# Optimization experiments

Measured on AMD Instinct MI355X. Metric: run time of the kernel, lower is better.

## Reference

```python
import jax, jax.numpy as jnp
import numpy as np

B, T_ENC, T_DEC = 64, 512, 400
IN_DIM, R = 80, 2
D_ENC, D_ATT, D_PRE = 256, 256, 128
NEG_INF = -1e9


def _gru(x, h, Wi, Wh, bi, bh):
    # PyTorch GRUCell math
    gi = x @ Wi + bi
    gh = h @ Wh + bh
    ir, iz, inn = jnp.split(gi, 3, axis=-1)
    hr, hz, hn = jnp.split(gh, 3, axis=-1)
    r = jax.nn.sigmoid(ir + hr)
    z = jax.nn.sigmoid(iz + hz)
    n = jnp.tanh(inn + r * hn)
    return (1.0 - z) * n + z * h


def setup_inputs() -> dict:
    key = jax.random.key(0)
    ks = jax.random.split(key, 32)
    s = 0.05
    d_in = IN_DIM * R
    inp = {
        "encoder_outputs": jax.random.normal(ks[0], (B, T_ENC, D_ENC), jnp.float32),
        "inputs": jax.random.normal(ks[1], (B, T_DEC, d_in), jnp.float32),
        "memory_lengths": jax.random.randint(ks[2], (B,), T_ENC // 2, T_ENC + 1).astype(jnp.int32),
        # prenet
        "pre_W1": s * jax.random.normal(ks[3], (d_in, 256), jnp.float32),
        "pre_b1": jnp.zeros((256,), jnp.float32),
        "pre_W2": s * jax.random.normal(ks[4], (256, 128), jnp.float32),
        "pre_b2": jnp.zeros((128,), jnp.float32),
        # Bahdanau attention
        "mem_W": s * jax.random.normal(ks[5], (D_ENC, D_ATT), jnp.float32),
        "q_W": s * jax.random.normal(ks[6], (256, D_ATT), jnp.float32),
        "v_W": s * jax.random.normal(ks[7], (D_ATT, 1), jnp.float32),
        # attention GRUCell: input = cat(prenet 128, attention 256) = 384
        "att_Wi": s * jax.random.normal(ks[8], (384, 768), jnp.float32),
        "att_Wh": s * jax.random.normal(ks[9], (256, 768), jnp.float32),
        "att_bi": jnp.zeros((768,), jnp.float32),
        "att_bh": jnp.zeros((768,), jnp.float32),
        # project_to_decoder_in
        "proj_in_W": s * jax.random.normal(ks[10], (512, 256), jnp.float32),
        "proj_in_b": jnp.zeros((256,), jnp.float32),
        # decoder GRUCells
        "dec1_Wi": s * jax.random.normal(ks[11], (256, 768), jnp.float32),
        "dec1_Wh": s * jax.random.normal(ks[12], (256, 768), jnp.float32),
        "dec1_bi": jnp.zeros((768,), jnp.float32),
        "dec1_bh": jnp.zeros((768,), jnp.float32),
        "dec2_Wi": s * jax.random.normal(ks[13], (256, 768), jnp.float32),
        "dec2_Wh": s * jax.random.normal(ks[14], (256, 768), jnp.float32),
        "dec2_bi": jnp.zeros((768,), jnp.float32),
        "dec2_bh": jnp.zeros((768,), jnp.float32),
        # output projections
        "mel_W": s * jax.random.normal(ks[15], (256, d_in), jnp.float32),
        "mel_b": jnp.zeros((d_in,), jnp.float32),
        "gate_W": s * jax.random.normal(ks[16], (256, R), jnp.float32),
        "gate_b": jnp.zeros((R,), jnp.float32),
    }
    return inp


def _decoder_forward(encoder_outputs, inputs, memory_lengths,
                     pre_W1, pre_b1, pre_W2, pre_b2,
                     mem_W, q_W, v_W,
                     att_Wi, att_Wh, att_bi, att_bh,
                     proj_in_W, proj_in_b,
                     dec1_Wi, dec1_Wh, dec1_bi, dec1_bh,
                     dec2_Wi, dec2_Wh, dec2_bi, dec2_bh,
                     mel_W, mel_b, gate_W, gate_b):
    Bq, Tq, _ = encoder_outputs.shape
    processed_memory = encoder_outputs @ mem_W  # (B, T_enc, D_att)
    valid = jnp.arange(Tq)[None, :] < memory_lengths[:, None]  # (B, T_enc)

    # teacher forcing: input at step t is inputs[t-1], zeros at t=0
    prev = jnp.concatenate([jnp.zeros_like(inputs[:, :1]), inputs[:, :-1]], axis=1)
    prev = jnp.swapaxes(prev, 0, 1)  # (T_dec, B, in_dim*r)

    def prenet(x):
        # dropout is identity in eval mode
        h = jax.nn.relu(x @ pre_W1 + pre_b1)
        return jax.nn.relu(h @ pre_W2 + pre_b2)

    def step(carry, x_prev):
        att_h, h1, h2, cur_att = carry
        pre = prenet(x_prev)  # (B, 128)
        cell_in = jnp.concatenate([pre, cur_att], axis=-1)  # (B, 384)
        att_h = _gru(cell_in, att_h, att_Wi, att_Wh, att_bi, att_bh)  # (B, 256)
        # Bahdanau alignment over encoder memory
        score = jnp.squeeze(
            jnp.tanh(processed_memory + (att_h @ q_W)[:, None, :]) @ v_W, -1)  # (B, T_enc)
        score = jnp.where(valid, score, NEG_INF)
        align = jax.nn.softmax(score, axis=-1)
        cur_att = jnp.einsum('bt,btd->bd', align, encoder_outputs)  # (B, 256)
        dec_in = jnp.concatenate([att_h, cur_att], axis=-1) @ proj_in_W + proj_in_b
        h1 = _gru(dec_in, h1, dec1_Wi, dec1_Wh, dec1_bi, dec1_bh)
        d = h1 + dec_in
        h2 = _gru(d, h2, dec2_Wi, dec2_Wh, dec2_bi, dec2_bh)
        d = h2 + d
        gate = jax.nn.sigmoid(d @ gate_W + gate_b)  # (B, r)
        out = d @ mel_W + mel_b  # (B, in_dim*r)
        return (att_h, h1, h2, cur_att), (out, align, gate)

    z = jnp.zeros((Bq, 256), encoder_outputs.dtype)
    init = (z, z, z, z)
    _, (outs, aligns, gates) = jax.lax.scan(step, init, prev)
    outputs = jnp.swapaxes(outs, 0, 1)      # (B, T_dec, in_dim*r)
    alignments = jnp.swapaxes(aligns, 0, 1)  # (B, T_dec, T_enc)
    gates = jnp.swapaxes(gates, 0, 1)        # (B, T_dec, r)
    return outputs, alignments, gates


def reference(encoder_outputs, inputs, memory_lengths,
              pre_W1, pre_b1, pre_W2, pre_b2,
              mem_W, q_W, v_W,
              att_Wi, att_Wh, att_bi, att_bh,
              proj_in_W, proj_in_b,
              dec1_Wi, dec1_Wh, dec1_bi, dec1_bh,
              dec2_Wi, dec2_Wh, dec2_bi, dec2_bh,
              mel_W, mel_b, gate_W, gate_b):
    return _decoder_forward(encoder_outputs, inputs, memory_lengths,
                            pre_W1, pre_b1, pre_W2, pre_b2,
                            mem_W, q_W, v_W,
                            att_Wi, att_Wh, att_bi, att_bh,
                            proj_in_W, proj_in_b,
                            dec1_Wi, dec1_Wh, dec1_bi, dec1_bh,
                            dec2_Wi, dec2_Wh, dec2_bi, dec2_bh,
                            mel_W, mel_b, gate_W, gate_b)
```

## Files before the change

kernel.cpp:

```cpp
#include <hip/hip_runtime.h>

#define TDEC 400
#define NTH 512
#define NWG 256

typedef float f32x4 __attribute__((ext_vector_type(4)));
typedef unsigned u32x4 __attribute__((ext_vector_type(4)));
typedef unsigned u32x2 __attribute__((ext_vector_type(2)));

#define OFF_BAR   0
#define OFF_ATTH  11264
#define OFF_H1    44032
#define OFF_H2    76800
#define OFF_CURP  109568
#define OFF_ATTS  125952
#define OFF_Q     126208
#define ZERO_FLOATS 142592
#define OFF_D1    142592
#define OFF_SUMS  158976
#define OFF_C1    184576
#define OFF_PRE   185600
#define OFF_PMB   1824000
#define OFF_ENCB  6018304
#define OFF_D2A   10212608
#define T_WIT_A   10212608
#define T_WHT_A   10507520
#define T_M1T     10704128
#define T_WHT1    11097344
#define T_PJT     11293952
#define T_WIT2    11425024
#define T_WHT2    11621632
#define T_QWT     11818240
#define T_M1      11883776
#define OFF_BLOB  16766208

#define BLOB_N   26112
#define BLOB_STR 26624
#define BO_AI  0
#define BO_AH  4608
#define BO_Q   7680
#define BO_M1  8704
#define BO_H1  14848
#define BO_PJ  17920
#define BO_I2  19968
#define BO_H2  23040

#define AOFF 4096000
#define GOFF 17203200

#define MSTI  (8*1024)
#define GENI  (9*1024)
#define FAILI (10*1024)

__device__ __forceinline__ float fsig(float x){ return 1.0f/(1.0f+__expf(-x)); }
__device__ __forceinline__ float ftanh(float x){ float e = __expf(2.0f*x); return 1.0f - 2.0f/(e+1.0f); }
__device__ __forceinline__ float blo(unsigned u){ return __uint_as_float(u<<16); }
__device__ __forceinline__ float bhi(unsigned u){ return __uint_as_float(u & 0xffff0000u); }

__device__ __forceinline__ f32x4 cload16(const float* p){
  f32x4 r;
  asm volatile("global_load_dwordx4 %0, %1, off sc0 sc1" : "=v"(r) : "v"(p));
  return r;
}
__device__ __forceinline__ u32x4 cload16u(const unsigned short* p){
  u32x4 r;
  asm volatile("global_load_dwordx4 %0, %1, off sc0 sc1" : "=v"(r) : "v"(p));
  return r;
}
__device__ __forceinline__ float aload4(const float* p){
  unsigned u = __hip_atomic_load((const unsigned*)p, __ATOMIC_RELAXED, __HIP_MEMORY_SCOPE_AGENT);
  return __uint_as_float(u);
}
__device__ __forceinline__ void astore4(float* p, float v){
  __hip_atomic_store((unsigned*)p, __float_as_uint(v), __ATOMIC_RELAXED, __HIP_MEMORY_SCOPE_AGENT);
}
__device__ __forceinline__ void aadd(float* p, float v){
  __hip_atomic_fetch_add(p, v, __ATOMIC_RELAXED, __HIP_MEMORY_SCOPE_AGENT);
}
__device__ __forceinline__ int aloadi(const int* p){
  return __hip_atomic_load(p, __ATOMIC_RELAXED, __HIP_MEMORY_SCOPE_AGENT);
}

__device__ __forceinline__ void ldsbar(){
  __builtin_amdgcn_sched_barrier(0);
  asm volatile("s_waitcnt lgkmcnt(0)" ::: "memory");
  __builtin_amdgcn_s_barrier();
  __builtin_amdgcn_sched_barrier(0);
}

__device__ __forceinline__ void gbar(int* bar, int g, int l, int n){
  asm volatile("s_waitcnt vmcnt(0)" ::: "memory");
  __syncthreads();
  if (threadIdx.x == 0){
    if (aloadi(&bar[FAILI]) == 0){
      int a = __hip_atomic_fetch_add(&bar[(l&7)*1024 + g*64], 1, __ATOMIC_RELAXED, __HIP_MEMORY_SCOPE_AGENT);
      if (a == 8*n - 1){
        int m = __hip_atomic_fetch_add(&bar[MSTI + g*64], 1, __ATOMIC_RELAXED, __HIP_MEMORY_SCOPE_AGENT);
        if (m == 8*n - 1)
          __hip_atomic_store(&bar[GENI + g*64], n, __ATOMIC_RELAXED, __HIP_MEMORY_SCOPE_AGENT);
      }
      int sp = 0;
      while (aloadi(&bar[GENI + g*64]) < n){
        __builtin_amdgcn_s_sleep(1);
        if (++sp > (1<<20)){
          __hip_atomic_store(&bar[FAILI], 1, __ATOMIC_RELAXED, __HIP_MEMORY_SCOPE_AGENT);
          break;
        }
      }
    }
  }
  __syncthreads();
}

__device__ __forceinline__ unsigned short f2bf(float f){
  unsigned u = __float_as_uint(f);
  return (unsigned short)((u + 0x7fffu + ((u>>16)&1u)) >> 16);
}

template<int N8>
__device__ __forceinline__ float bdot(const unsigned short* wr, const float* xr){
  f32x4 accA = 0.f, accB = 0.f;
  #pragma unroll 4
  for (int k = 0; k < N8; ++k){
    u32x4 u = *(const u32x4*)(wr + k*8);
    f32x4 a = *(const f32x4*)(xr + k*8);
    f32x4 b = *(const f32x4*)(xr + k*8 + 4);
    f32x4 w0, w1;
    w0[0]=blo(u[0]); w0[1]=bhi(u[0]); w0[2]=blo(u[1]); w0[3]=bhi(u[1]);
    w1[0]=blo(u[2]); w1[1]=bhi(u[2]); w1[2]=blo(u[3]); w1[3]=bhi(u[3]);
    accA += w0*a; accB += w1*b;
  }
  f32x4 s = accA + accB;
  return s[0]+s[1]+s[2]+s[3];
}

__global__ __launch_bounds__(256, 1) void transpose_k(const float* __restrict__ in,
                                                      float* __restrict__ outp, int K, int C){
  __shared__ float tl[32][33];
  int c0 = blockIdx.x * 32, k0 = blockIdx.y * 32;
  int tx = threadIdx.x & 31, ty = threadIdx.x >> 5;
  for (int i = ty; i < 32; i += 8){
    int k = k0 + i, c = c0 + tx;
    if (k < K && c < C) tl[i][tx] = in[k * C + c];
  }
  __syncthreads();
  for (int i = ty; i < 32; i += 8){
    int c = c0 + i, k = k0 + tx;
    if (c < C && k < K) outp[c * K + k] = tl[tx][i];
  }
}

__global__ __launch_bounds__(128, 1) void fuse_k(const float* __restrict__ projW,
    const float* __restrict__ d1Wi, float* __restrict__ M1){
  int jt = blockIdx.x % 6, i = blockIdx.x / 6;
  int j = jt * 128 + threadIdx.x;
  float acc = 0.f;
  for (int k = 0; k < 256; ++k) acc += projW[i*256+k] * d1Wi[k*768+j];
  M1[i*768+j] = acc;
}

__global__ __launch_bounds__(256, 1) void c1_k(const float* __restrict__ projB,
    const float* __restrict__ d1Wi, const float* __restrict__ d1Bi, float* __restrict__ C1){
  int j = blockIdx.x * 256 + threadIdx.x;
  float acc = d1Bi[j];
  for (int k = 0; k < 256; ++k) acc += projB[k] * d1Wi[k*768+j];
  C1[j] = acc;
}

__global__ __launch_bounds__(512, 1) void pack_k(float* __restrict__ ws){
  int sl = blockIdx.x;
  const float* TAI = ws + T_WIT_A;
  const float* TAH = ws + T_WHT_A;
  const float* TM1 = ws + T_M1T;
  const float* TH1 = ws + T_WHT1;
  const float* TPJ = ws + T_PJT;
  const float* TI2 = ws + T_WIT2;
  const float* TH2 = ws + T_WHT2;
  const float* TQ  = ws + T_QWT;
  unsigned short* blob = (unsigned short*)(ws + OFF_BLOB) + (size_t)sl * BLOB_STR;
  for (int idx = threadIdx.x; idx < BLOB_N; idx += 512){
    float v; int cs, k, o;
    if (idx < BO_AH){ cs = idx / 384; k = idx - cs*384;
      v = TAI[((cs%3)*256 + sl*4 + cs/3)*384 + k]; }
    else if (idx < BO_Q){ o = idx - BO_AH; cs = o >> 8; k = o & 255;
      v = TAH[((cs%3)*256 + sl*4 + cs/3)*256 + k]; }
    else if (idx < BO_M1){ o = idx - BO_Q; cs = o >> 8; k = o & 255;
      v = TQ[(sl*4 + cs)*256 + k]; }
    else if (idx < BO_H1){ o = idx - BO_M1; cs = o >> 9; k = o & 511;
      v = TM1[((cs%3)*256 + sl*4 + cs/3)*512 + k]; }
    else if (idx < BO_PJ){ o = idx - BO_H1; cs = o >> 8; k = o & 255;
      v = TH1[((cs%3)*256 + sl*4 + cs/3)*256 + k]; }
    else if (idx < BO_I2){ o = idx - BO_PJ; cs = o >> 9; k = o & 511;
      v = TPJ[(sl*4 + cs)*512 + k]; }
    else if (idx < BO_H2){ o = idx - BO_I2; cs = o >> 8; k = o & 255;
      v = TI2[((cs%3)*256 + sl*4 + cs/3)*256 + k]; }
    else { o = idx - BO_H2; cs = o >> 8; k = o & 255;
      v = TH2[((cs%3)*256 + sl*4 + cs/3)*256 + k]; }
    blob[idx] = f2bf(v);
  }
}

__global__ __launch_bounds__(256, 1) void qt_k(const float* __restrict__ ws,
                                               float* __restrict__ out){
  unsigned short* qtb = (unsigned short*)(out + GOFF);
  const float* TQ = ws + T_QWT;
  int idx = blockIdx.x * 256 + threadIdx.x;
  int it = idx >> 11, j = (idx >> 3) & 255, e = idx & 7;
  qtb[idx] = f2bf(TQ[j*256 + it*8 + e]);
}

__global__ __launch_bounds__(NTH, 1) void prenet_k(float* __restrict__ ws,
    const float* __restrict__ inp, const float* __restrict__ W1, const float* __restrict__ B1,
    const float* __restrict__ W2, const float* __restrict__ B2){
  __shared__ float xT[160 * 33];
  __shared__ float hT[256 * 33];
  int t = blockIdx.x, half = blockIdx.y, tid = threadIdx.x;
  int bbase = half * 32;
  for (int r = tid; r < 32 * 160; r += NTH){
    int b2 = r / 160; int k = r - b2 * 160;
    xT[k * 33 + b2] = (t == 0) ? 0.f : inp[((bbase + b2) * TDEC + (t - 1)) * 160 + k];
  }
  __syncthreads();
  int bl = tid & 31, slot = tid >> 5;
  float acc1[16];
  #pragma unroll
  for (int i = 0; i < 16; ++i) acc1[i] = 0.f;
  for (int k = 0; k < 160; ++k){
    float xv = xT[k * 33 + bl];
    const float* wr = W1 + k * 256 + slot * 16;
    #pragma unroll
    for (int i = 0; i < 16; ++i) acc1[i] += xv * wr[i];
  }
  #pragma unroll
  for (int i = 0; i < 16; ++i){
    int c = slot * 16 + i;
    hT[c * 33 + bl] = fmaxf(acc1[i] + B1[c], 0.f);
  }
  __syncthreads();
  float acc2[8];
  #pragma unroll
  for (int i = 0; i < 8; ++i) acc2[i] = 0.f;
  for (int k = 0; k < 256; ++k){
    float hv = hT[k * 33 + bl];
    const float* wr = W2 + k * 128 + slot * 8;
    #pragma unroll
    for (int i = 0; i < 8; ++i) acc2[i] += hv * wr[i];
  }
  unsigned short* dst = (unsigned short*)(ws + OFF_PRE) + (size_t)t*8192 + (bbase + bl)*128 + slot*8;
  u32x4 pk;
  #pragma unroll
  for (int i = 0; i < 4; ++i){
    float v0 = fmaxf(acc2[2*i] + B2[slot*8 + 2*i], 0.f);
    float v1 = fmaxf(acc2[2*i+1] + B2[slot*8 + 2*i+1], 0.f);
    pk[i] = (unsigned)f2bf(v0) | ((unsigned)f2bf(v1) << 16);
  }
  *(u32x4*)dst = pk;
}

__global__ __launch_bounds__(NTH, 1) void pm_k(float* __restrict__ ws,
    const float* __restrict__ enc, const float* __restrict__ memW){
  int wg = blockIdx.x, tid = threadIdx.x;
  int b = wg & 63, th = wg >> 6;
  int slot = tid & 7, tt = tid >> 3;
  int trow = th * 64 + tt;
  const float* er = enc + ((size_t)(b * 512 + trow)) * 256;
  f32x4 acc[8];
  #pragma unroll
  for (int i = 0; i < 8; ++i) acc[i] = 0.f;
  for (int k = 0; k < 256; ++k){
    float ev = er[k];
    const f32x4* wr = (const f32x4*)(memW + k * 256 + slot * 32);
    #pragma unroll
    for (int i = 0; i < 8; ++i) acc[i] += ev * wr[i];
  }
  unsigned short* pmB = (unsigned short*)(ws + OFF_PMB);
  unsigned short* dst = pmB + ((size_t)(b * 512 + trow)) * 256 + slot * 32;
  #pragma unroll
  for (int i = 0; i < 8; ++i){
    u32x2 pk;
    pk[0] = (unsigned)f2bf(acc[i][0]) | ((unsigned)f2bf(acc[i][1]) << 16);
    pk[1] = (unsigned)f2bf(acc[i][2]) | ((unsigned)f2bf(acc[i][3]) << 16);
    *(u32x2*)(dst + i * 4) = pk;
  }
  const float* e2 = enc + ((size_t)(b * 512 + th * 64)) * 256;
  unsigned* eb = (unsigned*)((unsigned short*)(ws + OFF_ENCB) + ((size_t)(b * 512 + th * 64)) * 256);
  for (int i = tid; i < 64 * 128; i += NTH){
    float v0 = e2[i * 2], v1 = e2[i * 2 + 1];
    eb[i] = (unsigned)f2bf(v0) | ((unsigned)f2bf(v1) << 16);
  }
}

__global__ __launch_bounds__(NTH, 2) void decoder_k(
    float* __restrict__ ws, float* __restrict__ out,
    const int* __restrict__ memlen,
    const float* __restrict__ vW,
    const float* __restrict__ attBi, const float* __restrict__ attBh,
    const float* __restrict__ projB,
    const float* __restrict__ d1Bh,
    const float* __restrict__ d2Bi, const float* __restrict__ d2Bh)
{
  const int wg = blockIdx.x, tid = threadIdx.x;
  int* bar = (int*)ws;
  float* attH = ws + OFF_ATTH;
  float* h1a  = ws + OFF_H1;
  float* h2a  = ws + OFF_H2;
  float* const curB[2]  = { ws + OFF_CURP, ws + OFF_Q };
  float* const attSB[2] = { ws + OFF_ATTS, ws + OFF_ATTS + 64 };
  float* d1v  = ws + OFF_D1;
  const float* C1v = ws + OFF_C1;
  const unsigned short* preB16 = (const unsigned short*)(ws + OFF_PRE);
  const unsigned short* pmB  = (const unsigned short*)(ws + OFF_PMB);
  const unsigned short* encB = (const unsigned short*)(ws + OFF_ENCB);
  const unsigned short* qtb = (const unsigned short*)(out + GOFF);
  float* d2a  = ws + OFF_D2A;

  __shared__ float POOL[16128];
  float* const ahL  = POOL;
  float* const cnL  = POOL + 4160;
  float* const h1L  = POOL + 8320;
  float* const xpre = POOL + 12480;
  float* const dL   = POOL;
  float* const h2L  = POOL + 4160;
  float* const ctxP = POOL + 8320;
  float* const qIn  = POOL + 12416;
  float* const ewGi  = POOL + 14592;
  float* const ewGh  = POOL + 14784;
  float* const ewGi2 = POOL + 14976;
  float* const ewGh2 = POOL + 15168;
  float* const pdec  = POOL + 15360;
  float* const qL    = POOL + 15488;
  float* const vL    = POOL + 15744;
  float* const eL    = POOL + 16000;

  if (tid < 256) vL[tid] = vW[tid];

  const int g = wg >> 6, l = wg & 63;
  const int sl = l;
  const int b0 = g << 4;
  const int b2 = b0 + (l >> 2), ch2 = l & 3;
  const int len2 = memlen[b2];
  const unsigned short* blob = (const unsigned short*)(ws + OFF_BLOB) + (size_t)sl * BLOB_STR;

  const int bq = tid & 15, x = tid >> 4;
  const int cs = (x >= 12 && x < 24) ? (x - 12) : x;
  const int gg = cs % 3, jh = cs / 3;
  const int col = gg * 256 + sl * 4 + jh;

  const int r0 = tid >> 6, c0 = (tid & 63) << 2;
  const int r1 = r0 + 8;
  const int prr = tid >> 4, pcc = (tid & 15) * 8;

  float rb0 = 0.f, rb1 = 0.f, rb2 = 0.f;
  if (x < 12){ rb0 = attBi[col]; rb1 = C1v[col];  rb2 = d2Bi[col]; }
  else if (x < 24){ rb0 = attBh[col]; rb1 = d1Bh[col]; rb2 = d2Bh[col]; }
  float pjB2 = 0.f;
  if (tid >= 64 && tid < 128) pjB2 = projB[sl*4 + ((tid - 64) >> 4)];

  u32x4 pmv[8], env[8];
  {
    int te = tid >> 2, part = tid & 3;
    const u32x4* pmp = (const u32x4*)(pmB + ((size_t)(b2*512 + ch2*128 + te))*256 + part*64);
    #pragma unroll
    for (int i = 0; i < 8; ++i) pmv[i] = pmp[i];
    int ich = tid >> 5, dblk = tid & 31;
    const unsigned short* ep = encB + ((size_t)(b2*512 + ch2*128 + ich*8))*256 + dblk*8;
    #pragma unroll
    for (int i = 0; i < 8; ++i) env[i] = *(const u32x4*)(ep + i*256);
  }

  f32x4 eA0, eA1, eH0, eH1;
  u32x4 ppre = 0u;
  eA0 = cload16(attH + 16384 + ((b0+r0)<<8) + c0);
  eA1 = cload16(attH + 16384 + ((b0+r1)<<8) + c0);
  eH0 = cload16(h1a + ((b0+r0)<<8) + c0);
  eH1 = cload16(h1a + ((b0+r1)<<8) + c0);
  if (tid < 256) ppre = cload16u(preB16 + (b0 + prr)*128 + pcc);

  int bn = 0;
  for (int t = -1; t <= 400; ++t){
    const int w = t & 1, wn = w ^ 1;

    if (t >= 0){
      const bool doP2 = (t < 400), doP5 = (t >= 1);
      f32x4 vD0 = cload16(d1v + ((b0+r0)<<8) + c0);
      f32x4 vD1 = cload16(d1v + ((b0+r1)<<8) + c0);
      f32x4 vH0 = cload16(h2a + w*16384 + ((b0+r0)<<8) + c0);
      f32x4 vH1 = cload16(h2a + w*16384 + ((b0+r1)<<8) + c0);
      f32x4 qv = 0.f;
      if (tid < 64) qv = cload16(attH + w*16384 + b2*256 + tid*4);
      eA0 = cload16(attH + w*16384 + ((b0+r0)<<8) + c0);
      eA1 = cload16(attH + w*16384 + ((b0+r1)<<8) + c0);
      eH0 = cload16(h1a + wn*16384 + ((b0+r0)<<8) + c0);
      eH1 = cload16(h1a + wn*16384 + ((b0+r1)<<8) + c0);
      {
        int tn = (t + 1 < TDEC) ? (t + 1) : (TDEC - 1);
        if (tid < 256) ppre = cload16u(preB16 + (size_t)tn*8192 + (b0 + prr)*128 + pcc);
      }
      asm volatile("s_waitcnt vmcnt(0)" : "+v"(vD0),"+v"(vD1),"+v"(vH0),"+v"(vH1),"+v"(qv));
      __builtin_amdgcn_sched_barrier(0);
      if (tid < 64) *(f32x4*)(qIn + tid*4) = qv;
      *(f32x4*)(dL + r0*260 + c0) = vD0;  *(f32x4*)(dL + r1*260 + c0) = vD1;
      *(f32x4*)(h2L + r0*260 + c0) = vH0; *(f32x4*)(h2L + r1*260 + c0) = vH1;
      ldsbar();
      if (doP2){
        int lane = tid & 63;
        int j = (tid >> 6)*32 + (lane & 31), hf = lane >> 5;
        const unsigned short* qw = qtb + j*8 + (size_t)hf*32768;
        const float* qx = qIn + hf*128;
        f32x4 aA = 0.f, aB = 0.f;
        #pragma unroll 4
        for (int it = 0; it < 16; ++it){
          u32x4 u = *(const u32x4*)(qw + (size_t)it*2048);
          f32x4 a = *(const f32x4*)(qx + it*8);
          f32x4 b = *(const f32x4*)(qx + it*8 + 4);
          f32x4 w0, w1;
          w0[0]=blo(u[0]); w0[1]=bhi(u[0]); w0[2]=blo(u[1]); w0[3]=bhi(u[1]);
          w1[0]=blo(u[2]); w1[1]=bhi(u[2]); w1[2]=blo(u[3]); w1[3]=bhi(u[3]);
          aA += w0*a; aB += w1*b;
        }
        f32x4 s4 = aA + aB;
        float s = s4[0]+s4[1]+s4[2]+s4[3];
        s += __shfl_xor(s, 32);
        if (hf == 0) qL[j] = s;
      }
      if (doP5){
        if (x < 12)
          ewGi[cs*16 + bq] = bdot<32>(blob + BO_I2 + cs*256, dL + bq*260) + rb2;
        else if (x < 24)
          ewGh[cs*16 + bq] = bdot<32>(blob + BO_H2 + cs*256, h2L + bq*260) + rb2;
      }
      ldsbar();
      if (doP2){
        int te = tid >> 2, part = tid & 3;
        int ge = ch2*128 + te;
        float a4 = 0.f;
        #pragma unroll
        for (int i = 0; i < 8; ++i){
          u32x4 u = pmv[i];
          int kb = part*64 + i*8;
          a4 += ftanh(blo(u[0]) + qL[kb+0]) * vL[kb+0];
          a4 += ftanh(bhi(u[0]) + qL[kb+1]) * vL[kb+1];
          a4 += ftanh(blo(u[1]) + qL[kb+2]) * vL[kb+2];
          a4 += ftanh(bhi(u[1]) + qL[kb+3]) * vL[kb+3];
          a4 += ftanh(blo(u[2]) + qL[kb+4]) * vL[kb+4];
          a4 += ftanh(bhi(u[2]) + qL[kb+5]) * vL[kb+5];
          a4 += ftanh(blo(u[3]) + qL[kb+6]) * vL[kb+6];
          a4 += ftanh(bhi(u[3]) + qL[kb+7]) * vL[kb+7];
        }
        a4 += __shfl_xor(a4, 1);
        a4 += __shfl_xor(a4, 2);
        float e = (ge < len2) ? __expf(a4) : 0.f;
        if (part == 0){
          eL[te] = e;
          out[AOFF + ((size_t)(b2*TDEC + t))*512 + ge] = e;
        }
      }
      if (doP5 && tid < 64){
        int bt = tid & 15, jj = tid >> 4;
        int j = sl*4 + jj;
        float ir = ewGi[(jj*3+0)*16+bt] + ewGh[(jj*3+0)*16+bt];
        float iz = ewGi[(jj*3+1)*16+bt] + ewGh[(jj*3+1)*16+bt];
        float inn = ewGi[(jj*3+2)*16+bt];
        float hn  = ewGh[(jj*3+2)*16+bt];
        float rg = fsig(ir), z = fsig(iz);
        float n = ftanh(inn + rg * hn);
        float hv = h2L[bt*260 + j];
        float hnew = (1.f - z)*n + z*hv;
        astore4(h2a + wn*16384 + (b0+bt)*256 + j, hnew);
        d2a[(size_t)(t-1)*16384 + j*64 + (b0+bt)] = hnew + dL[bt*260 + j];
      }
      ldsbar();
      if (doP2){
        if (tid < 64){
          float s = eL[tid] + eL[tid + 64];
          #pragma unroll
          for (int o = 32; o > 0; o >>= 1) s += __shfl_down(s, o);
          if (tid == 0) aadd(attSB[w] + b2, s);
        }
        {
          int ich = tid >> 5, dblk = tid & 31;
          f32x4 acA = 0.f, acB = 0.f;
          #pragma unroll
          for (int i = 0; i < 8; ++i){
            u32x4 u = env[i];
            float e = eL[ich*8 + i];
            acA[0] += e*blo(u[0]); acA[1] += e*bhi(u[0]);
            acA[2] += e*blo(u[1]); acA[3] += e*bhi(u[1]);
            acB[0] += e*blo(u[2]); acB[1] += e*bhi(u[2]);
            acB[2] += e*blo(u[3]); acB[3] += e*bhi(u[3]);
          }
          *(f32x4*)(ctxP + tid*8) = acA;
          *(f32x4*)(ctxP + tid*8 + 4) = acB;
        }
      }
      ldsbar();
      if (doP2 && tid < 256){
        int dblk = tid >> 3, d = tid & 7;
        float s = 0.f;
        #pragma unroll
        for (int i = 0; i < 16; ++i) s += ctxP[i*256 + dblk*8 + d];
        aadd(curB[w] + b2*256 + dblk*8 + d, s);
      }
    }

    gbar(bar, g, l, ++bn);
    if (t == 400) break;

    {
      const bool doP0 = (t <= 398), doP4 = (t >= 0);
      f32x4 vC0 = cload16(curB[w] + ((b0+r0)<<8) + c0);
      f32x4 vC1 = cload16(curB[w] + ((b0+r1)<<8) + c0);
      float s0 = aload4(attSB[w] + b0 + r0), s1 = aload4(attSB[w] + b0 + r1);
      asm volatile("s_waitcnt vmcnt(0)" : "+v"(vC0),"+v"(vC1));
      __builtin_amdgcn_sched_barrier(0);
      float iv0 = s0 > 0.f ? 1.f/s0 : 0.f, iv1 = s1 > 0.f ? 1.f/s1 : 0.f;
      *(f32x4*)(ahL + r0*260 + c0) = eA0; *(f32x4*)(ahL + r1*260 + c0) = eA1;
      *(f32x4*)(h1L + r0*260 + c0) = eH0; *(f32x4*)(h1L + r1*260 + c0) = eH1;
      *(f32x4*)(cnL + r0*260 + c0) = vC0*iv0; *(f32x4*)(cnL + r1*260 + c0) = vC1*iv1;
      if (tid < 256){
        float* xd = xpre + prr*132 + pcc;
        xd[0]=blo(ppre[0]); xd[1]=bhi(ppre[0]); xd[2]=blo(ppre[1]); xd[3]=bhi(ppre[1]);
        xd[4]=blo(ppre[2]); xd[5]=bhi(ppre[2]); xd[6]=blo(ppre[3]); xd[7]=bhi(ppre[3]);
      }
      if (tid < 64) astore4(curB[wn] + wg*64 + tid, 0.f);
      if (sl == 0 && tid < 16) astore4(attSB[wn] + b0 + tid, 0.f);
      if (t >= 0 && sl == 0 && tid < 16)
        ws[OFF_SUMS + t*64 + b0 + tid] = aload4(attSB[w] + b0 + tid);
      ldsbar();
      if (x < 12){
        if (doP0)
          ewGi[cs*16 + bq] = bdot<16>(blob + BO_AI + cs*384, xpre + bq*132)
                           + bdot<32>(blob + BO_AI + cs*384 + 128, cnL + bq*260) + rb0;
        if (doP4)
          ewGi2[cs*16 + bq] = bdot<32>(blob + BO_M1 + cs*512, ahL + bq*260)
                            + bdot<32>(blob + BO_M1 + cs*512 + 256, cnL + bq*260) + rb1;
      } else if (x < 24){
        if (doP0)
          ewGh[cs*16 + bq] = bdot<32>(blob + BO_AH + cs*256, ahL + bq*260) + rb0;
        if (doP4)
          ewGh2[cs*16 + bq] = bdot<32>(blob + BO_H1 + cs*256, h1L + bq*260) + rb1;
      } else if (doP4){
        int idx = tid - 384;
        int bq2 = idx & 15, cc = (idx >> 4) & 3, half = idx >> 6;
        pdec[idx] = bdot<32>(blob + BO_PJ + cc*512 + half*256, (half ? cnL : ahL) + bq2*260);
      }
      ldsbar();
      if (doP0 && tid < 64){
        int bt = tid & 15, jj = tid >> 4;
        int j = sl*4 + jj;
        float ir = ewGi[(jj*3+0)*16+bt] + ewGh[(jj*3+0)*16+bt];
        float iz = ewGi[(jj*3+1)*16+bt] + ewGh[(jj*3+1)*16+bt];
        float inn = ewGi[(jj*3+2)*16+bt];
        float hn  = ewGh[(jj*3+2)*16+bt];
        float rg = fsig(ir), z = fsig(iz);
        float n = ftanh(inn + rg * hn);
        float h = ahL[bt*260 + j];
        astore4(attH + wn*16384 + (b0+bt)*256 + j, (1.f - z)*n + z*h);
      }
      if (doP4 && tid >= 64 && tid < 128){
        int t2 = tid - 64;
        int bt = t2 & 15, jj = t2 >> 4;
        int j = sl*4 + jj;
        float ir = ewGi2[(jj*3+0)*16+bt] + ewGh2[(jj*3+0)*16+bt];
        float iz = ewGi2[(jj*3+1)*16+bt] + ewGh2[(jj*3+1)*16+bt];
        float inn = ewGi2[(jj*3+2)*16+bt];
        float hn  = ewGh2[(jj*3+2)*16+bt];
        float rg = fsig(ir), z = fsig(iz);
        float n = ftanh(inn + rg * hn);
        float hv = h1L[bt*260 + j];
        float hnew = (1.f - z)*n + z*hv;
        float dec = pdec[jj*16 + bt] + pdec[64 + jj*16 + bt] + pjB2;
        astore4(h1a + w*16384 + (b0+bt)*256 + j, hnew);
        astore4(d1v + (b0+bt)*256 + j, hnew + dec);
      }
    }
    gbar(bar, g, l, ++bn);
  }
}

__global__ __launch_bounds__(NTH, 1) void rescale_k(const float* __restrict__ ws,
                                                    float* __restrict__ out){
  int blk = blockIdx.x;
  int b = blk / TDEC, t = blk - b * TDEC;
  float s = ws[OFF_SUMS + t*64 + b];
  float inv = (s > 0.f) ? 1.f/s : 0.f;
  out[AOFF + (size_t)blk*512 + threadIdx.x] *= inv;
}

__global__ __launch_bounds__(NTH, 1) void outproj_k(const float* __restrict__ ws,
    float* __restrict__ out, const float* __restrict__ melW, const float* __restrict__ melB,
    const float* __restrict__ gateW, const float* __restrict__ gateB){
  int t = blockIdx.x, tid = threadIdx.x;
  int cx = tid & 255, bh = tid >> 8;
  const float* src = ws + OFF_D2A + t*16384 + bh*32;
  float acc[32];
  #pragma unroll
  for (int i = 0; i < 32; ++i) acc[i] = 0.f;
  bool ismel = (cx < 160);
  bool isgate = (cx >= 160 && cx < 162);
  for (int j = 0; j < 256; ++j){
    float wv = 0.f;
    if (ismel) wv = melW[j*160 + cx];
    else if (isgate) wv = gateW[j*2 + (cx - 160)];
    const f32x4* dp = (const f32x4*)(src + j*64);
    f32x4 vv[8];
    #pragma unroll
    for (int q = 0; q < 8; ++q) vv[q] = dp[q];
    #pragma unroll
    for (int q = 0; q < 8; ++q){
      acc[q*4+0] += vv[q][0]*wv; acc[q*4+1] += vv[q][1]*wv;
      acc[q*4+2] += vv[q][2]*wv; acc[q*4+3] += vv[q][3]*wv;
    }
  }
  if (ismel){
    float bb = melB[cx];
    #pragma unroll
    for (int i = 0; i < 32; ++i){
      int b = bh*32 + i;
      out[((size_t)(b*TDEC + t))*160 + cx] = acc[i] + bb;
    }
  } else if (isgate){
    int g = cx - 160;
    float bb = gateB[g];
    #pragma unroll
    for (int i = 0; i < 32; ++i){
      int b = bh*32 + i;
      out[GOFF + ((size_t)(b*TDEC + t))*2 + g] = fsig(acc[i] + bb);
    }
  }
}

extern "C" void kernel_launch(void* const* d_in, const int* in_sizes, int n_in,
                              void* d_out, int out_size, void* d_ws, size_t ws_size,
                              hipStream_t stream)
{
  (void)in_sizes; (void)n_in; (void)out_size; (void)ws_size;
  const float* enc   = (const float*)d_in[0];
  const float* inp   = (const float*)d_in[1];
  const int*   mlen  = (const int*)d_in[2];
  const float* preW1 = (const float*)d_in[3];
  const float* preB1 = (const float*)d_in[4];
  const float* preW2 = (const float*)d_in[5];
  const float* preB2 = (const float*)d_in[6];
  const float* memW  = (const float*)d_in[7];
  const float* qW    = (const float*)d_in[8];
  const float* vW    = (const float*)d_in[9];
  const float* attWi = (const float*)d_in[10];
  const float* attWh = (const float*)d_in[11];
  const float* attBi = (const float*)d_in[12];
  const float* attBh = (const float*)d_in[13];
  const float* projW = (const float*)d_in[14];
  const float* projB = (const float*)d_in[15];
  const float* d1Wi  = (const float*)d_in[16];
  const float* d1Wh  = (const float*)d_in[17];
  const float* d1Bi  = (const float*)d_in[18];
  const float* d1Bh  = (const float*)d_in[19];
  const float* d2Wi  = (const float*)d_in[20];
  const float* d2Wh  = (const float*)d_in[21];
  const float* d2Bi  = (const float*)d_in[22];
  const float* d2Bh  = (const float*)d_in[23];
  const float* melW  = (const float*)d_in[24];
  const float* melB  = (const float*)d_in[25];
  const float* gateW = (const float*)d_in[26];
  const float* gateB = (const float*)d_in[27];
  float* ws = (float*)d_ws;
  float* out = (float*)d_out;

  hipMemsetAsync(d_ws, 0, (size_t)ZERO_FLOATS * sizeof(float), stream);

  dim3 tt(256);
  transpose_k<<<dim3(24, 12), tt, 0, stream>>>(attWi, ws + T_WIT_A, 384, 768);
  transpose_k<<<dim3(24, 8),  tt, 0, stream>>>(attWh, ws + T_WHT_A, 256, 768);
  transpose_k<<<dim3(24, 8),  tt, 0, stream>>>(d1Wh,  ws + T_WHT1, 256, 768);
  transpose_k<<<dim3(24, 8),  tt, 0, stream>>>(d2Wi,  ws + T_WIT2, 256, 768);
  transpose_k<<<dim3(24, 8),  tt, 0, stream>>>(d2Wh,  ws + T_WHT2, 256, 768);
  transpose_k<<<dim3(8, 16),  tt, 0, stream>>>(projW, ws + T_PJT, 512, 256);
  transpose_k<<<dim3(8, 8),   tt, 0, stream>>>(qW,    ws + T_QWT, 256, 256);
  fuse_k<<<3072, 128, 0, stream>>>(projW, d1Wi, ws + T_M1);
  c1_k<<<3, 256, 0, stream>>>(projB, d1Wi, d1Bi, ws + OFF_C1);
  transpose_k<<<dim3(24, 16), tt, 0, stream>>>(ws + T_M1, ws + T_M1T, 512, 768);
  pack_k<<<64, NTH, 0, stream>>>(ws);
  qt_k<<<256, 256, 0, stream>>>(ws, out);

  prenet_k<<<dim3(TDEC, 2), NTH, 0, stream>>>(ws, inp, preW1, preB1, preW2, preB2);
  pm_k<<<512, NTH, 0, stream>>>(ws, enc, memW);
  decoder_k<<<NWG, NTH, 0, stream>>>(ws, out, mlen, vW, attBi, attBh, projB,
                                     d1Bh, d2Bi, d2Bh);
  rescale_k<<<64 * TDEC, NTH, 0, stream>>>(ws, out);
  outproj_k<<<TDEC, NTH, 0, stream>>>(ws, out, melW, melB, gateW, gateB);
}
```

Before: 12.02 ms.

## Restructure grid barrier into 16 counters with leader flag polling, cache query weights in registers

Replaces the two-level grid barrier (8 counters plus a master counter) with 16 per-slice counters. Each counter sets a flag, and a single leader workgroup polls all 16 flags before publishing the generation. This is meant to shorten the serial atomic chain on the critical path of the persistent kernel's per-step barrier. The query-projection weights are also preloaded once into registers instead of being reloaded every timestep, and the prenet loads drop the cache-bypass bits. The cost is 64 more VGPRs per thread, which risks spills or lower occupancy, and barrier latency now depends on one leader workgroup.

Result: slower. 23.68 ms (+97.0%).

```diff
diff --git a/kernel.cpp b/kernel.cpp
--- a/kernel.cpp
+++ b/kernel.cpp
@@ -48,8 +48,8 @@
 #define AOFF 4096000
 #define GOFF 17203200
 
-#define MSTI  (8*1024)
-#define GENI  (9*1024)
+#define FLAGB (8*1024)
+#define GENIB 9728
 #define FAILI (10*1024)
 
 __device__ __forceinline__ float fsig(float x){ return 1.0f/(1.0f+__expf(-x)); }
@@ -62,9 +62,9 @@
   asm volatile("global_load_dwordx4 %0, %1, off sc0 sc1" : "=v"(r) : "v"(p));
   return r;
 }
-__device__ __forceinline__ u32x4 cload16u(const unsigned short* p){
+__device__ __forceinline__ u32x4 ncload16u(const unsigned short* p){
   u32x4 r;
-  asm volatile("global_load_dwordx4 %0, %1, off sc0 sc1" : "=v"(r) : "v"(p));
+  asm volatile("global_load_dwordx4 %0, %1, off" : "=v"(r) : "v"(p));
   return r;
 }
 __device__ __forceinline__ float aload4(const float* p){
@@ -79,6 +79,9 @@
 }
 __device__ __forceinline__ int aloadi(const int* p){
   return __hip_atomic_load(p, __ATOMIC_RELAXED, __HIP_MEMORY_SCOPE_AGENT);
+}
+__device__ __forceinline__ void astorei(int* p, int v){
+  __hip_atomic_store(p, v, __ATOMIC_RELAXED, __HIP_MEMORY_SCOPE_AGENT);
 }
 
 __device__ __forceinline__ void ldsbar(){
@@ -93,18 +96,33 @@
   __syncthreads();
   if (threadIdx.x == 0){
     if (aloadi(&bar[FAILI]) == 0){
-      int a = __hip_atomic_fetch_add(&bar[(l&7)*1024 + g*64], 1, __ATOMIC_RELAXED, __HIP_MEMORY_SCOPE_AGENT);
-      if (a == 8*n - 1){
-        int m = __hip_atomic_fetch_add(&bar[MSTI + g*64], 1, __ATOMIC_RELAXED, __HIP_MEMORY_SCOPE_AGENT);
-        if (m == 8*n - 1)
-          __hip_atomic_store(&bar[GENI + g*64], n, __ATOMIC_RELAXED, __HIP_MEMORY_SCOPE_AGENT);
-      }
-      int sp = 0;
-      while (aloadi(&bar[GENI + g*64]) < n){
-        __builtin_amdgcn_s_sleep(1);
-        if (++sp > (1<<20)){
-          __hip_atomic_store(&bar[FAILI], 1, __ATOMIC_RELAXED, __HIP_MEMORY_SCOPE_AGENT);
-          break;
+      int c = l & 15;
+      int a = __hip_atomic_fetch_add(&bar[c*512 + g*64], 1, __ATOMIC_RELAXED, __HIP_MEMORY_SCOPE_AGENT);
+      if (a == 4*n - 1)
+        astorei(&bar[FLAGB + g*64 + c], n);
+      if (l == 0){
+        int sp = 0;
+        for (;;){
+          int ok = 1;
+          #pragma unroll
+          for (int c2 = 0; c2 < 16; ++c2)
+            ok &= (aloadi(&bar[FLAGB + g*64 + c2]) >= n) ? 1 : 0;
+          if (ok) break;
+          __builtin_amdgcn_s_sleep(1);
+          if (++sp > (1<<20)){
+            astorei(&bar[FAILI], 1);
+            break;
+          }
+        }
+        astorei(&bar[GENIB + g*64], n);
+      } else {
+        int sp = 0;
+        while (aloadi(&bar[GENIB + g*64]) < n){
+          __builtin_amdgcn_s_sleep(1);
+          if (++sp > (1<<20)){
+            astorei(&bar[FAILI], 1);
+            break;
+          }
         }
       }
     }
@@ -356,7 +374,7 @@
   float pjB2 = 0.f;
   if (tid >= 64 && tid < 128) pjB2 = projB[sl*4 + ((tid - 64) >> 4)];
 
-  u32x4 pmv[8], env[8];
+  u32x4 pmv[8], env[8], qwv[16];
   {
     int te = tid >> 2, part = tid & 3;
     const u32x4* pmp = (const u32x4*)(pmB + ((size_t)(b2*512 + ch2*128 + te))*256 + part*64);
@@ -366,7 +384,14 @@
     const unsigned short* ep = encB + ((size_t)(b2*512 + ch2*128 + ich*8))*256 + dblk*8;
     #pragma unroll
     for (int i = 0; i < 8; ++i) env[i] = *(const u32x4*)(ep + i*256);
-  }
+    int lane = tid & 63;
+    int jq = (tid >> 6)*32 + (lane & 31), hfq = lane >> 5;
+    const unsigned short* qw = qtb + jq*8 + (size_t)hfq*32768;
+    #pragma unroll
+    for (int it = 0; it < 16; ++it) qwv[it] = *(const u32x4*)(qw + (size_t)it*2048);
+  }
+  const int qhf = (tid & 63) >> 5;
+  const int qj  = (tid >> 6)*32 + (tid & 31);
 
   f32x4 eA0, eA1, eH0, eH1;
   u32x4 ppre = 0u;
@@ -374,7 +399,7 @@
   eA1 = cload16(attH + 16384 + ((b0+r1)<<8) + c0);
   eH0 = cload16(h1a + ((b0+r0)<<8) + c0);
   eH1 = cload16(h1a + ((b0+r1)<<8) + c0);
-  if (tid < 256) ppre = cload16u(preB16 + (b0 + prr)*128 + pcc);
+  if (tid < 256) ppre = ncload16u(preB16 + (b0 + prr)*128 + pcc);
 
   int bn = 0;
   for (int t = -1; t <= 400; ++t){
@@ -394,7 +419,7 @@
       eH1 = cload16(h1a + wn*16384 + ((b0+r1)<<8) + c0);
       {
         int tn = (t + 1 < TDEC) ? (t + 1) : (TDEC - 1);
-        if (tid < 256) ppre = cload16u(preB16 + (size_t)tn*8192 + (b0 + prr)*128 + pcc);
+        if (tid < 256) ppre = ncload16u(preB16 + (size_t)tn*8192 + (b0 + prr)*128 + pcc);
       }
       asm volatile("s_waitcnt vmcnt(0)" : "+v"(vD0),"+v"(vD1),"+v"(vH0),"+v"(vH1),"+v"(qv));
       __builtin_amdgcn_sched_barrier(0);
@@ -403,14 +428,11 @@
       *(f32x4*)(h2L + r0*260 + c0) = vH0; *(f32x4*)(h2L + r1*260 + c0) = vH1;
       ldsbar();
       if (doP2){
-        int lane = tid & 63;
-        int j = (tid >> 6)*32 + (lane & 31), hf = lane >> 5;
-        const unsigned short* qw = qtb + j*8 + (size_t)hf*32768;
-        const float* qx = qIn + hf*128;
+        const float* qx = qIn + qhf*128;
         f32x4 aA = 0.f, aB = 0.f;
-        #pragma unroll 4
+        #pragma unroll
         for (int it = 0; it < 16; ++it){
-          u32x4 u = *(const u32x4*)(qw + (size_t)it*2048);
+          u32x4 u = qwv[it];
           f32x4 a = *(const f32x4*)(qx + it*8);
           f32x4 b = *(const f32x4*)(qx + it*8 + 4);
           f32x4 w0, w1;
@@ -421,7 +443,7 @@
         f32x4 s4 = aA + aB;
         float s = s4[0]+s4[1]+s4[2]+s4[3];
         s += __shfl_xor(s, 32);
-        if (hf == 0) qL[j] = s;
+        if (qhf == 0) qL[qj] = s;
       }
       if (doP5){
         if (x < 12)
```
